# Kernel optimization log

Measured on AMD Instinct MI355X. Metric: run time of the kernel, lower is better.

## Reference

```python
import jax, jax.numpy as jnp
import numpy as np


def setup_inputs() -> dict:
    key = jax.random.key(0)
    k1, k2, k3, k4 = jax.random.split(key, 4)
    b, c, h, w = 4, 256, 64, 64
    Fq_l = jax.random.normal(k1, (b, c, h, w), dtype=jnp.float32)
    Fp_l = jax.random.normal(k2, (b, c, h, w), dtype=jnp.float32)
    # 1x1 conv: weight [out=c//2, in=c], bias [c//2]
    W = jax.random.normal(k3, (c // 2, c), dtype=jnp.float32) * (1.0 / np.sqrt(c))
    bias = jax.random.normal(k4, (c // 2,), dtype=jnp.float32) * 0.01
    return {"Fq_l": Fq_l, "Fp_l": Fp_l, "W": W, "bias": bias}


def reference(Fq_l, Fp_l, W, bias):
    b, c, h, w = Fq_l.shape
    hw = h * w
    # 1x1 conv == per-pixel linear projection
    q = jnp.einsum('oc,bchw->bohw', W, Fq_l) + bias[None, :, None, None]
    p = jnp.einsum('oc,bchw->bohw', W, Fp_l) + bias[None, :, None, None]
    qf = q.reshape(b, -1, hw)  # [b, c/2, hw]
    pf = p.reshape(b, -1, hw)
    qf = qf / jnp.linalg.norm(qf, axis=1, keepdims=True)
    pf = pf / jnp.linalg.norm(pf, axis=1, keepdims=True)
    # cosine similarity, [b, hw, hw]
    sim = jnp.einsum('bcn,bcm->bnm', qf, pf)
    idx = jnp.argmax(sim, axis=-1)  # [b, hw]
    Fp_flat = Fp_l.reshape(b, c, hw)
    aligned = jnp.take_along_axis(Fp_flat, idx[:, None, :], axis=2)  # [b, c, hw]
    return aligned.reshape(b, c, h, w)
```

## Files before the change

kernel.cpp:

```cpp
#include <hip/hip_runtime.h>

#define HW 4096
#define BCAP 1024u
#define OCAP 65536u

typedef short bf16x8 __attribute__((ext_vector_type(8)));
typedef float f32x16 __attribute__((ext_vector_type(16)));

__device__ __forceinline__ ushort f2bf_rne(float f) {
    unsigned u = __float_as_uint(f);
    return (ushort)((u + 0x7FFFu + ((u >> 16) & 1u)) >> 16);
}

__global__ __launch_bounds__(256) void init_kernel(
    unsigned long long* __restrict__ best, unsigned* __restrict__ bcnt,
    unsigned* __restrict__ ocnt)
{
    int i = blockIdx.x * 256 + threadIdx.x;
    best[i] = 0ull;
    if (i < 512) bcnt[i] = 0u;
    if (i == 0) ocnt[0] = 0u;
}

__global__ __launch_bounds__(256) void transpose_w_kernel(
    const float* __restrict__ Wm, float* __restrict__ Wt)
{
    const int o = blockIdx.x;
    const int c = threadIdx.x;
    Wt[c * 128 + o] = Wm[o * 256 + c];
}

__global__ __launch_bounds__(256) void proj_kernel(
    const float* __restrict__ Fq, const float* __restrict__ Fp,
    const float* __restrict__ Wt, const float* __restrict__ bias,
    float* __restrict__ Qt, float* __restrict__ Pt,
    ushort* __restrict__ Qpk, ushort* __restrict__ Ppk,
    float* __restrict__ qnorm)
{
    __shared__ float Ws[64][128];
    __shared__ float Xs[64][64];
    __shared__ float psum[16][68];

    const int tid = threadIdx.x;
    const int z  = blockIdx.z;
    const float* __restrict__ X = z ? Fp : Fq;
    const int b  = blockIdx.y;
    const int n0 = blockIdx.x * 64;
    const int og = tid >> 4;
    const int ng = tid & 15;

    float acc[4][8];
    #pragma unroll
    for (int i = 0; i < 4; ++i)
        #pragma unroll
        for (int j = 0; j < 8; ++j) acc[i][j] = 0.f;

    for (int cc = 0; cc < 4; ++cc) {
        __syncthreads();
        {
            const float4* src = (const float4*)(Wt + (size_t)cc * 64 * 128);
            float4* dst = (float4*)Ws;
            #pragma unroll
            for (int it = 0; it < 8; ++it) dst[it * 256 + tid] = src[it * 256 + tid];
        }
        #pragma unroll
        for (int it = 0; it < 4; ++it) {
            int f = it * 256 + tid;
            int r = f >> 4, n4 = f & 15;
            *(float4*)&Xs[r][n4 * 4] =
                *(const float4*)&X[(size_t)(b * 256 + cc * 64 + r) * HW + n0 + n4 * 4];
        }
        __syncthreads();

        for (int r = 0; r < 64; ++r) {
            float4 w0 = *(const float4*)&Ws[r][og * 8];
            float4 w1 = *(const float4*)&Ws[r][og * 8 + 4];
            float4 xv = *(const float4*)&Xs[r][ng * 4];
            float wa[8] = {w0.x, w0.y, w0.z, w0.w, w1.x, w1.y, w1.z, w1.w};
            float xa[4] = {xv.x, xv.y, xv.z, xv.w};
            #pragma unroll
            for (int i = 0; i < 4; ++i)
                #pragma unroll
                for (int j = 0; j < 8; ++j)
                    acc[i][j] += wa[j] * xa[i];
        }
    }

    {
        float4 b0 = *(const float4*)&bias[og * 8];
        float4 b1 = *(const float4*)&bias[og * 8 + 4];
        float ba[8] = {b0.x, b0.y, b0.z, b0.w, b1.x, b1.y, b1.z, b1.w};
        #pragma unroll
        for (int i = 0; i < 4; ++i)
            #pragma unroll
            for (int j = 0; j < 8; ++j) acc[i][j] += ba[j];
    }

    #pragma unroll
    for (int i = 0; i < 4; ++i) {
        float s = 0.f;
        #pragma unroll
        for (int j = 0; j < 8; ++j) s += acc[i][j] * acc[i][j];
        psum[og][ng * 4 + i] = s;
    }
    __syncthreads();
    float tot[4];
    #pragma unroll
    for (int i = 0; i < 4; ++i) {
        float s = 0.f;
        #pragma unroll
        for (int g = 0; g < 16; ++g) s += psum[g][ng * 4 + i];
        tot[i] = s;
    }

    if (z) {
        #pragma unroll
        for (int i = 0; i < 4; ++i) {
            float s = 1.0f / sqrtf(tot[i]);
            #pragma unroll
            for (int j = 0; j < 8; ++j) acc[i][j] *= s;
        }
    } else if (og == 0) {
        #pragma unroll
        for (int i = 0; i < 4; ++i)
            qnorm[b * HW + n0 + ng * 4 + i] = sqrtf(tot[i]);
    }

    {
        float* __restrict__ T = z ? Pt : Qt;
        #pragma unroll
        for (int i = 0; i < 4; ++i) {
            size_t tb = ((size_t)b * HW + n0 + ng * 4 + i) * 128 + og * 8;
            *(float4*)&T[tb]     = make_float4(acc[i][0], acc[i][1], acc[i][2], acc[i][3]);
            *(float4*)&T[tb + 4] = make_float4(acc[i][4], acc[i][5], acc[i][6], acc[i][7]);
        }
    }
    {
        ushort* __restrict__ PK = z ? Ppk : Qpk;
        const int ks = og >> 1;
        #pragma unroll
        for (int i = 0; i < 4; ++i) {
            const int na  = n0 + ng * 4 + i;
            const int t32 = na >> 5;
            const int lt  = (na & 31) + 32 * (og & 1);
            ushort u[8];
            #pragma unroll
            for (int k = 0; k < 8; ++k) u[k] = f2bf_rne(acc[i][k]);
            size_t pk = ((((size_t)b * 128 + t32) * 8 + ks) * 64 + lt) * 8;
            uint4 w;
            w.x = (unsigned)u[0] | ((unsigned)u[1] << 16);
            w.y = (unsigned)u[2] | ((unsigned)u[3] << 16);
            w.z = (unsigned)u[4] | ((unsigned)u[5] << 16);
            w.w = (unsigned)u[6] | ((unsigned)u[7] << 16);
            *(uint4*)&PK[pk] = w;
        }
    }
}

__global__ __launch_bounds__(256, 2) void sim_max_kernel(
    const ushort* __restrict__ Qpk, const ushort* __restrict__ Ppk,
    float* __restrict__ Vmax)
{
    __shared__ ushort Qs[16384];
    __shared__ ushort Bs[16384];

    const int tid  = threadIdx.x;
    const int lane = tid & 63;
    const int w    = tid >> 6;
    const int nb   = blockIdx.x;
    const int b    = blockIdx.y;
    const int ms   = blockIdx.z;

    {
        const uint4* src = (const uint4*)(Qpk + ((size_t)b * 128 + nb * 4) * 4096);
        uint4* dst = (uint4*)Qs;
        #pragma unroll
        for (int it = 0; it < 8; ++it) dst[it * 256 + tid] = src[it * 256 + tid];
    }

    float bestv[16];
    #pragma unroll
    for (int r = 0; r < 16; ++r) bestv[r] = -1e30f;

    for (int ch = 0; ch < 8; ++ch) {
        __syncthreads();
        {
            const uint4* src = (const uint4*)(Ppk +
                ((size_t)b * 128 + ms * 32 + ch * 4) * 4096);
            uint4* dst = (uint4*)Bs;
            #pragma unroll
            for (int it = 0; it < 8; ++it) dst[it * 256 + tid] = src[it * 256 + tid];
        }
        __syncthreads();

        for (int mtl = 0; mtl < 4; ++mtl) {
            f32x16 acc;
            #pragma unroll
            for (int r = 0; r < 16; ++r) acc[r] = 0.f;
            #pragma unroll
            for (int ks = 0; ks < 8; ++ks) {
                bf16x8 a  = *(const bf16x8*)&Qs[((w   * 8 + ks) * 64 + lane) * 8];
                bf16x8 bb = *(const bf16x8*)&Bs[((mtl * 8 + ks) * 64 + lane) * 8];
                acc = __builtin_amdgcn_mfma_f32_32x32x16_bf16(a, bb, acc, 0, 0, 0);
            }
            #pragma unroll
            for (int r = 0; r < 16; ++r)
                bestv[r] = fmaxf(bestv[r], acc[r]);
        }
    }

    #pragma unroll
    for (int r = 0; r < 16; ++r) {
        float v = bestv[r];
        #pragma unroll
        for (int d = 1; d < 32; d <<= 1)
            v = fmaxf(v, __shfl_xor(v, d, 64));
        if ((lane & 31) == 0) {
            int nl_ = (r & 3) + 8 * (r >> 2) + 4 * (lane >> 5);
            int na = nb * 128 + w * 32 + nl_;
            Vmax[((size_t)b * HW + na) * 4 + ms] = v;
        }
    }
}

__global__ __launch_bounds__(256, 2) void sim_emit_kernel(
    const ushort* __restrict__ Qpk, const ushort* __restrict__ Ppk,
    const float* __restrict__ thr,
    unsigned* __restrict__ cand, unsigned* __restrict__ bcnt,
    unsigned* __restrict__ ocand, unsigned* __restrict__ ocnt)
{
    __shared__ ushort Qs[16384];
    __shared__ ushort Bs[16384];
    __shared__ unsigned lds_cand[BCAP];
    __shared__ unsigned lds_cnt;

    const int tid  = threadIdx.x;
    const int lane = tid & 63;
    const int w    = tid >> 6;
    const int nb   = blockIdx.x;
    const int b    = blockIdx.y;
    const int ms   = blockIdx.z;
    const int blk  = nb + 32 * (b + 4 * ms);

    if (tid == 0) lds_cnt = 0u;

    {
        const uint4* src = (const uint4*)(Qpk + ((size_t)b * 128 + nb * 4) * 4096);
        uint4* dst = (uint4*)Qs;
        #pragma unroll
        for (int it = 0; it < 8; ++it) dst[it * 256 + tid] = src[it * 256 + tid];
    }

    float thrreg[16];
    #pragma unroll
    for (int r = 0; r < 16; ++r) {
        int nl_ = (r & 3) + 8 * (r >> 2) + 4 * (lane >> 5);
        thrreg[r] = thr[b * HW + nb * 128 + w * 32 + nl_];
    }

    for (int ch = 0; ch < 8; ++ch) {
        __syncthreads();
        {
            const uint4* src = (const uint4*)(Ppk +
                ((size_t)b * 128 + ms * 32 + ch * 4) * 4096);
            uint4* dst = (uint4*)Bs;
            #pragma unroll
            for (int it = 0; it < 8; ++it) dst[it * 256 + tid] = src[it * 256 + tid];
        }
        __syncthreads();

        for (int mtl = 0; mtl < 4; ++mtl) {
            f32x16 acc;
            #pragma unroll
            for (int r = 0; r < 16; ++r) acc[r] = 0.f;
            #pragma unroll
            for (int ks = 0; ks < 8; ++ks) {
                bf16x8 a  = *(const bf16x8*)&Qs[((w   * 8 + ks) * 64 + lane) * 8];
                bf16x8 bb = *(const bf16x8*)&Bs[((mtl * 8 + ks) * 64 + lane) * 8];
                acc = __builtin_amdgcn_mfma_f32_32x32x16_bf16(a, bb, acc, 0, 0, 0);
            }

            const int m = ms * 1024 + ch * 128 + mtl * 32 + (lane & 31);
            #pragma unroll
            for (int r = 0; r < 16; ++r) {
                if (acc[r] >= thrreg[r]) {
                    int nl_ = (r & 3) + 8 * (r >> 2) + 4 * (lane >> 5);
                    int na = nb * 128 + w * 32 + nl_;
                    unsigned enc = ((unsigned)b << 24) | ((unsigned)na << 12) | (unsigned)m;
                    unsigned pos = atomicAdd(&lds_cnt, 1u);
                    if (pos < BCAP) {
                        lds_cand[pos] = enc;
                    } else {
                        unsigned op = atomicAdd(ocnt, 1u);
                        if (op < OCAP) ocand[op] = enc;
                    }
                }
            }
        }
    }

    __syncthreads();
    unsigned cnt = lds_cnt;
    if (cnt > BCAP) cnt = BCAP;
    for (unsigned i = tid; i < cnt; i += 256)
        cand[(size_t)blk * BCAP + i] = lds_cand[i];
    if (tid == 0) bcnt[blk] = cnt;
}

__global__ __launch_bounds__(256) void thresh_kernel(
    const float* __restrict__ Vmax, const float* __restrict__ qnorm,
    float* __restrict__ thr)
{
    int i = blockIdx.x * 256 + threadIdx.x;
    float g = -1e30f;
    #pragma unroll
    for (int s = 0; s < 4; ++s) g = fmaxf(g, Vmax[(size_t)i * 4 + s]);
    thr[i] = g - (0.016f * qnorm[i] + 1e-6f);
}

__device__ __forceinline__ void rescore_one(
    const float* __restrict__ Qt, const float* __restrict__ Pt,
    unsigned c, unsigned long long* __restrict__ best)
{
    int m = c & 0xFFF, n = (c >> 12) & 0xFFF, b = c >> 24;
    const float* __restrict__ q = Qt + ((size_t)b * HW + n) * 128;
    const float* __restrict__ p = Pt + ((size_t)b * HW + m) * 128;
    float acc = 0.f;
    for (int k = 0; k < 128; ++k) acc += q[k] * p[k];
    unsigned u = __float_as_uint(acc);
    unsigned kk = (u & 0x80000000u) ? ~u : (u | 0x80000000u);
    unsigned long long key = ((unsigned long long)kk << 32) | (unsigned)(4095 - m);
    atomicMax(&best[(size_t)b * HW + n], key);
}

__global__ __launch_bounds__(256) void rescore_kernel(
    const float* __restrict__ Qt, const float* __restrict__ Pt,
    const unsigned* __restrict__ cand, const unsigned* __restrict__ bcnt,
    const unsigned* __restrict__ ocand, const unsigned* __restrict__ ocnt,
    unsigned long long* __restrict__ best)
{
    const int blk = blockIdx.x;
    const int tid = threadIdx.x;
    unsigned cnt = bcnt[blk];
    for (unsigned i = tid; i < cnt; i += 256)
        rescore_one(Qt, Pt, cand[(size_t)blk * BCAP + i], best);

    unsigned total = ocnt[0];
    if (total > OCAP) total = OCAP;
    for (unsigned i = blk * 256 + tid; i < total; i += 512 * 256)
        rescore_one(Qt, Pt, ocand[i], best);
}

__global__ __launch_bounds__(256) void gather_kernel(
    const float* __restrict__ Fp, const unsigned long long* __restrict__ best,
    float* __restrict__ out)
{
    __shared__ float row[4096];
    const int blk = blockIdx.x;
    const int c = blk & 255;
    const int b = blk >> 8;
    const int tid = threadIdx.x;

    const float* __restrict__ src = Fp + ((size_t)b * 256 + c) * HW;
    #pragma unroll
    for (int it = 0; it < 4; ++it) {
        int f = it * 256 + tid;
        *(float4*)&row[f * 4] = *(const float4*)&src[f * 4];
    }
    __syncthreads();

    float* __restrict__ dst = out + ((size_t)b * 256 + c) * HW;
    #pragma unroll
    for (int it = 0; it < 16; ++it) {
        int n = it * 256 + tid;
        int m = 4095 - (int)(best[(size_t)b * HW + n] & 0xFFFull);
        dst[n] = row[m];
    }
}

extern "C" void kernel_launch(void* const* d_in, const int* in_sizes, int n_in,
                              void* d_out, int out_size, void* d_ws, size_t ws_size,
                              hipStream_t stream) {
    const float* Fq   = (const float*)d_in[0];
    const float* Fp   = (const float*)d_in[1];
    const float* Wm   = (const float*)d_in[2];
    const float* bias = (const float*)d_in[3];
    float* out = (float*)d_out;

    char* base = (char*)d_ws;
    float*  Qt    = (float*)(base);
    float*  Pt    = (float*)(base + (8u << 20));
    ushort* Qpk   = (ushort*)(base + (16u << 20));
    ushort* Ppk   = (ushort*)(base + (20u << 20));
    char* x = base + (24u << 20);
    float*  qnorm = (float*)x;              x += 65536;
    float*  Vmax  = (float*)x;              x += 262144;
    float*  thr   = (float*)x;              x += 65536;
    unsigned long long* best = (unsigned long long*)x; x += 131072;
    unsigned* bcnt = (unsigned*)x;          x += 4096;
    unsigned* ocnt = (unsigned*)x;          x += 16;
    unsigned* cand = (unsigned*)x;          x += (size_t)512 * BCAP * 4;
    unsigned* ocand = (unsigned*)x;         x += OCAP * 4;
    float*  Wtg   = (float*)x;

    init_kernel<<<64, 256, 0, stream>>>(best, bcnt, ocnt);
    transpose_w_kernel<<<128, 256, 0, stream>>>(Wm, Wtg);
    proj_kernel<<<dim3(64, 4, 2), 256, 0, stream>>>(Fq, Fp, Wtg, bias,
                                                    Qt, Pt, Qpk, Ppk, qnorm);
    sim_max_kernel<<<dim3(32, 4, 4), 256, 0, stream>>>(Qpk, Ppk, Vmax);
    thresh_kernel<<<64, 256, 0, stream>>>(Vmax, qnorm, thr);
    sim_emit_kernel<<<dim3(32, 4, 4), 256, 0, stream>>>(Qpk, Ppk, thr,
                                                        cand, bcnt, ocand, ocnt);
    rescore_kernel<<<512, 256, 0, stream>>>(Qt, Pt, cand, bcnt, ocand, ocnt, best);
    gather_kernel<<<1024, 256, 0, stream>>>(Fp, best, out);
}
```

Baseline: 180.4 us.

## Replace second similarity GEMM pass with stored column-group maxima scan

The max pass now also writes, for each 16-row group and column, a bf16 upper bound (rounded up) of the column's maximum similarity. A new scan kernel compares these against the group's minimum threshold to emit candidate columns, so the second full bf16 GEMM pass (sim_emit) is dropped. Rescoring then works per row group, with Q rows staged in LDS and each candidate column tested against all 16 rows, keeping only those above each row's threshold. This trades the second GEMM for an extra 8 MB Cmax write and read, plus a coarser candidate set that may hold more rescoring work per group.

```diff
diff --git a/kernel.cpp b/kernel.cpp
--- a/kernel.cpp
+++ b/kernel.cpp
@@ -1,7 +1,7 @@
 #include <hip/hip_runtime.h>
 
 #define HW 4096
-#define BCAP 1024u
+#define GCAP 512u
 #define OCAP 65536u
 
 typedef short bf16x8 __attribute__((ext_vector_type(8)));
@@ -12,13 +12,20 @@
     return (ushort)((u + 0x7FFFu + ((u >> 16) & 1u)) >> 16);
 }
 
+__device__ __forceinline__ ushort f2bf_up(float f) {
+    unsigned u = __float_as_uint(f);
+    ushort t = (ushort)(u >> 16);
+    if (!(u & 0x80000000u) && (u & 0xFFFFu)) t += 1;
+    return t;
+}
+
 __global__ __launch_bounds__(256) void init_kernel(
-    unsigned long long* __restrict__ best, unsigned* __restrict__ bcnt,
+    unsigned long long* __restrict__ best, unsigned* __restrict__ gcnt,
     unsigned* __restrict__ ocnt)
 {
     int i = blockIdx.x * 256 + threadIdx.x;
     best[i] = 0ull;
-    if (i < 512) bcnt[i] = 0u;
+    if (i < 1024) gcnt[i] = 0u;
     if (i == 0) ocnt[0] = 0u;
 }
 
@@ -159,7 +166,7 @@
 
 __global__ __launch_bounds__(256, 2) void sim_max_kernel(
     const ushort* __restrict__ Qpk, const ushort* __restrict__ Ppk,
-    float* __restrict__ Vmax)
+    float* __restrict__ Vmax, ushort* __restrict__ Cmax)
 {
     __shared__ ushort Qs[16384];
     __shared__ ushort Bs[16384];
@@ -178,6 +185,9 @@
         for (int it = 0; it < 8; ++it) dst[it * 256 + tid] = src[it * 256 + tid];
     }
 
+    const size_t crow = ((size_t)b * 256 + (size_t)(nb * 4 + w) * 2 + (lane >> 5)) * 4096;
+    const int mb0 = ms * 1024 + (lane & 31);
+
     float bestv[16];
     #pragma unroll
     for (int r = 0; r < 16; ++r) bestv[r] = -1e30f;
@@ -206,6 +216,12 @@
             #pragma unroll
             for (int r = 0; r < 16; ++r)
                 bestv[r] = fmaxf(bestv[r], acc[r]);
+
+            float c0 = fmaxf(fmaxf(fmaxf(acc[0], acc[1]), fmaxf(acc[2], acc[3])),
+                             fmaxf(fmaxf(acc[4], acc[5]), fmaxf(acc[6], acc[7])));
+            float c1 = fmaxf(fmaxf(fmaxf(acc[8], acc[9]), fmaxf(acc[10], acc[11])),
+                             fmaxf(fmaxf(acc[12], acc[13]), fmaxf(acc[14], acc[15])));
+            Cmax[crow + mb0 + ch * 128 + mtl * 32] = f2bf_up(fmaxf(c0, c1));
         }
     }
 
@@ -223,76 +239,66 @@
     }
 }
 
-__global__ __launch_bounds__(256, 2) void sim_emit_kernel(
-    const ushort* __restrict__ Qpk, const ushort* __restrict__ Ppk,
-    const float* __restrict__ thr,
-    unsigned* __restrict__ cand, unsigned* __restrict__ bcnt,
+__global__ __launch_bounds__(256) void thresh_kernel(
+    const float* __restrict__ Vmax, const float* __restrict__ qnorm,
+    float* __restrict__ thr, float* __restrict__ gmin)
+{
+    __shared__ float red[256];
+    const int tid = threadIdx.x;
+    int i = blockIdx.x * 256 + tid;
+    float g = -1e30f;
+    #pragma unroll
+    for (int s = 0; s < 4; ++s) g = fmaxf(g, Vmax[(size_t)i * 4 + s]);
+    float t = g - (0.016f * qnorm[i] + 1e-6f);
+    thr[i] = t;
+    red[tid] = t;
+    __syncthreads();
+    if (tid < 16) {
+        int tile = tid >> 1, gs = tid & 1;
+        float mn = 1e30f;
+        #pragma unroll
+        for (int j = 0; j < 16; ++j) {
+            int nl = (j & 3) + 8 * (j >> 2) + 4 * gs;
+            mn = fminf(mn, red[tile * 32 + nl]);
+        }
+        gmin[blockIdx.x * 16 + tid] = mn;
+    }
+}
+
+__global__ __launch_bounds__(256) void scan_kernel(
+    const ushort* __restrict__ Cmax, const float* __restrict__ gmin,
+    unsigned* __restrict__ cand2, unsigned* __restrict__ gcnt,
     unsigned* __restrict__ ocand, unsigned* __restrict__ ocnt)
 {
-    __shared__ ushort Qs[16384];
-    __shared__ ushort Bs[16384];
-    __shared__ unsigned lds_cand[BCAP];
-    __shared__ unsigned lds_cnt;
-
-    const int tid  = threadIdx.x;
-    const int lane = tid & 63;
-    const int w    = tid >> 6;
-    const int nb   = blockIdx.x;
-    const int b    = blockIdx.y;
-    const int ms   = blockIdx.z;
-    const int blk  = nb + 32 * (b + 4 * ms);
-
-    if (tid == 0) lds_cnt = 0u;
-
-    {
-        const uint4* src = (const uint4*)(Qpk + ((size_t)b * 128 + nb * 4) * 4096);
-        uint4* dst = (uint4*)Qs;
-        #pragma unroll
-        for (int it = 0; it < 8; ++it) dst[it * 256 + tid] = src[it * 256 + tid];
-    }
-
-    float thrreg[16];
-    #pragma unroll
-    for (int r = 0; r < 16; ++r) {
-        int nl_ = (r & 3) + 8 * (r >> 2) + 4 * (lane >> 5);
-        thrreg[r] = thr[b * HW + nb * 128 + w * 32 + nl_];
-    }
-
-    for (int ch = 0; ch < 8; ++ch) {
-        __syncthreads();
-        {
-            const uint4* src = (const uint4*)(Ppk +
-                ((size_t)b * 128 + ms * 32 + ch * 4) * 4096);
-            uint4* dst = (uint4*)Bs;
-            #pragma unroll
-            for (int it = 0; it < 8; ++it) dst[it * 256 + tid] = src[it * 256 + tid];
-        }
-        __syncthreads();
-
-        for (int mtl = 0; mtl < 4; ++mtl) {
-            f32x16 acc;
-            #pragma unroll
-            for (int r = 0; r < 16; ++r) acc[r] = 0.f;
-            #pragma unroll
-            for (int ks = 0; ks < 8; ++ks) {
-                bf16x8 a  = *(const bf16x8*)&Qs[((w   * 8 + ks) * 64 + lane) * 8];
-                bf16x8 bb = *(const bf16x8*)&Bs[((mtl * 8 + ks) * 64 + lane) * 8];
-                acc = __builtin_amdgcn_mfma_f32_32x32x16_bf16(a, bb, acc, 0, 0, 0);
-            }
-
-            const int m = ms * 1024 + ch * 128 + mtl * 32 + (lane & 31);
-            #pragma unroll
-            for (int r = 0; r < 16; ++r) {
-                if (acc[r] >= thrreg[r]) {
-                    int nl_ = (r & 3) + 8 * (r >> 2) + 4 * (lane >> 5);
-                    int na = nb * 128 + w * 32 + nl_;
-                    unsigned enc = ((unsigned)b << 24) | ((unsigned)na << 12) | (unsigned)m;
-                    unsigned pos = atomicAdd(&lds_cnt, 1u);
-                    if (pos < BCAP) {
-                        lds_cand[pos] = enc;
+    __shared__ unsigned lcnt;
+    const int fg = blockIdx.x;
+    const int tid = threadIdx.x;
+    if (tid == 0) lcnt = 0u;
+    __syncthreads();
+
+    const float gm = gmin[fg];
+    const ushort* __restrict__ row = Cmax + (size_t)fg * 4096;
+
+    #pragma unroll
+    for (int it = 0; it < 4; ++it) {
+        int m0 = (it * 256 + tid) * 4;
+        uint2 v = *(const uint2*)&row[m0];
+        unsigned wv[2] = {v.x, v.y};
+        #pragma unroll
+        for (int h = 0; h < 2; ++h) {
+            float f0 = __uint_as_float((wv[h] & 0xFFFFu) << 16);
+            float f1 = __uint_as_float(wv[h] & 0xFFFF0000u);
+            #pragma unroll
+            for (int q = 0; q < 2; ++q) {
+                float f = q ? f1 : f0;
+                if (f >= gm) {
+                    unsigned m = (unsigned)(m0 + h * 2 + q);
+                    unsigned pos = atomicAdd(&lcnt, 1u);
+                    if (pos < GCAP) {
+                        cand2[(size_t)fg * GCAP + pos] = m;
                     } else {
                         unsigned op = atomicAdd(ocnt, 1u);
-                        if (op < OCAP) ocand[op] = enc;
+                        if (op < OCAP) ocand[op] = ((unsigned)fg << 12) | m;
                     }
                 }
             }
@@ -300,55 +306,78 @@
     }
 
     __syncthreads();
-    unsigned cnt = lds_cnt;
-    if (cnt > BCAP) cnt = BCAP;
-    for (unsigned i = tid; i < cnt; i += 256)
-        cand[(size_t)blk * BCAP + i] = lds_cand[i];
-    if (tid == 0) bcnt[blk] = cnt;
-}
-
-__global__ __launch_bounds__(256) void thresh_kernel(
-    const float* __restrict__ Vmax, const float* __restrict__ qnorm,
-    float* __restrict__ thr)
-{
-    int i = blockIdx.x * 256 + threadIdx.x;
-    float g = -1e30f;
-    #pragma unroll
-    for (int s = 0; s < 4; ++s) g = fmaxf(g, Vmax[(size_t)i * 4 + s]);
-    thr[i] = g - (0.016f * qnorm[i] + 1e-6f);
-}
-
-__device__ __forceinline__ void rescore_one(
-    const float* __restrict__ Qt, const float* __restrict__ Pt,
-    unsigned c, unsigned long long* __restrict__ best)
-{
-    int m = c & 0xFFF, n = (c >> 12) & 0xFFF, b = c >> 24;
-    const float* __restrict__ q = Qt + ((size_t)b * HW + n) * 128;
-    const float* __restrict__ p = Pt + ((size_t)b * HW + m) * 128;
-    float acc = 0.f;
-    for (int k = 0; k < 128; ++k) acc += q[k] * p[k];
-    unsigned u = __float_as_uint(acc);
-    unsigned kk = (u & 0x80000000u) ? ~u : (u | 0x80000000u);
-    unsigned long long key = ((unsigned long long)kk << 32) | (unsigned)(4095 - m);
-    atomicMax(&best[(size_t)b * HW + n], key);
+    if (tid == 0) gcnt[fg] = lcnt < GCAP ? lcnt : GCAP;
 }
 
 __global__ __launch_bounds__(256) void rescore_kernel(
     const float* __restrict__ Qt, const float* __restrict__ Pt,
-    const unsigned* __restrict__ cand, const unsigned* __restrict__ bcnt,
+    const float* __restrict__ thr,
+    const unsigned* __restrict__ cand2, const unsigned* __restrict__ gcnt,
     const unsigned* __restrict__ ocand, const unsigned* __restrict__ ocnt,
     unsigned long long* __restrict__ best)
 {
-    const int blk = blockIdx.x;
+    __shared__ float Qs[16][132];
+    __shared__ float thr_s[16];
+    __shared__ int nlist[16];
+
+    const int fg = blockIdx.x;
     const int tid = threadIdx.x;
-    unsigned cnt = bcnt[blk];
-    for (unsigned i = tid; i < cnt; i += 256)
-        rescore_one(Qt, Pt, cand[(size_t)blk * BCAP + i], best);
+    const int b = fg >> 8, g = fg & 255, t = g >> 1, gs = g & 1;
+
+    if (tid < 16) {
+        int n = t * 32 + (tid & 3) + 8 * (tid >> 2) + 4 * gs;
+        nlist[tid] = n;
+        thr_s[tid] = thr[b * HW + n];
+    }
+    __syncthreads();
+    #pragma unroll
+    for (int it = 0; it < 2; ++it) {
+        int idx = it * 256 + tid;
+        int row = idx >> 5, c4 = (idx & 31) * 4;
+        *(float4*)&Qs[row][c4] =
+            *(const float4*)&Qt[((size_t)b * HW + nlist[row]) * 128 + c4];
+    }
+    __syncthreads();
+
+    unsigned cnt = gcnt[fg];
+    for (unsigned p = tid; p < cnt * 16u; p += 256) {
+        unsigned i = p >> 4, sub = p & 15;
+        int m = (int)cand2[(size_t)fg * GCAP + i];
+        const float4* __restrict__ pr = (const float4*)&Pt[((size_t)b * HW + m) * 128];
+        float acc = 0.f;
+        #pragma unroll
+        for (int k = 0; k < 32; ++k) {
+            float4 pv = pr[k];
+            float4 qv = *(const float4*)&Qs[sub][k * 4];
+            acc += qv.x * pv.x + qv.y * pv.y + qv.z * pv.z + qv.w * pv.w;
+        }
+        if (acc >= thr_s[sub]) {
+            unsigned u = __float_as_uint(acc);
+            unsigned kk = (u & 0x80000000u) ? ~u : (u | 0x80000000u);
+            unsigned long long key = ((unsigned long long)kk << 32) | (unsigned)(4095 - m);
+            atomicMax(&best[(size_t)b * HW + nlist[sub]], key);
+        }
+    }
 
     unsigned total = ocnt[0];
     if (total > OCAP) total = OCAP;
-    for (unsigned i = blk * 256 + tid; i < total; i += 512 * 256)
-        rescore_one(Qt, Pt, ocand[i], best);
+    for (unsigned i = blockIdx.x * 256 + tid; i < total; i += 1024 * 256) {
+        unsigned e = ocand[i];
+        unsigned fg2 = e >> 12, m = e & 4095u;
+        int b2 = fg2 >> 8, g2 = fg2 & 255, t2 = g2 >> 1, gs2 = g2 & 1;
+        const float* __restrict__ prow = &Pt[((size_t)b2 * HW + m) * 128];
+        #pragma unroll 1
+        for (int j = 0; j < 16; ++j) {
+            int n = t2 * 32 + (j & 3) + 8 * (j >> 2) + 4 * gs2;
+            const float* __restrict__ q = &Qt[((size_t)b2 * HW + n) * 128];
+            float acc = 0.f;
+            for (int k = 0; k < 128; ++k) acc += q[k] * prow[k];
+            unsigned u = __float_as_uint(acc);
+            unsigned kk = (u & 0x80000000u) ? ~u : (u | 0x80000000u);
+            unsigned long long key = ((unsigned long long)kk << 32) | (unsigned)(4095 - m);
+            atomicMax(&best[(size_t)b2 * HW + n], key);
+        }
+    }
 }
 
 __global__ __launch_bounds__(256) void gather_kernel(
@@ -392,25 +421,27 @@
     float*  Pt    = (float*)(base + (8u << 20));
     ushort* Qpk   = (ushort*)(base + (16u << 20));
     ushort* Ppk   = (ushort*)(base + (20u << 20));
-    char* x = base + (24u << 20);
+    ushort* Cmax  = (ushort*)(base + (24u << 20));
+    char* x = base + (32u << 20);
     float*  qnorm = (float*)x;              x += 65536;
     float*  Vmax  = (float*)x;              x += 262144;
     float*  thr   = (float*)x;              x += 65536;
+    float*  gmin  = (float*)x;              x += 4096;
     unsigned long long* best = (unsigned long long*)x; x += 131072;
-    unsigned* bcnt = (unsigned*)x;          x += 4096;
-    unsigned* ocnt = (unsigned*)x;          x += 16;
-    unsigned* cand = (unsigned*)x;          x += (size_t)512 * BCAP * 4;
+    unsigned* gcnt = (unsigned*)x;          x += 4096;
+    unsigned* ocnt = (unsigned*)x;          x += 4096;
+    unsigned* cand2 = (unsigned*)x;         x += (size_t)1024 * GCAP * 4;
     unsigned* ocand = (unsigned*)x;         x += OCAP * 4;
     float*  Wtg   = (float*)x;
 
-    init_kernel<<<64, 256, 0, stream>>>(best, bcnt, ocnt);
+    init_kernel<<<64, 256, 0, stream>>>(best, gcnt, ocnt);
     transpose_w_kernel<<<128, 256, 0, stream>>>(Wm, Wtg);
     proj_kernel<<<dim3(64, 4, 2), 256, 0, stream>>>(Fq, Fp, Wtg, bias,
                                                     Qt, Pt, Qpk, Ppk, qnorm);
-    sim_max_kernel<<<dim3(32, 4, 4), 256, 0, stream>>>(Qpk, Ppk, Vmax);
-    thresh_kernel<<<64, 256, 0, stream>>>(Vmax, qnorm, thr);
-    sim_emit_kernel<<<dim3(32, 4, 4), 256, 0, stream>>>(Qpk, Ppk, thr,
-                                                        cand, bcnt, ocand, ocnt);
-    rescore_kernel<<<512, 256, 0, stream>>>(Qt, Pt, cand, bcnt, ocand, ocnt, best);
+    sim_max_kernel<<<dim3(32, 4, 4), 256, 0, stream>>>(Qpk, Ppk, Vmax, Cmax);
+    thresh_kernel<<<64, 256, 0, stream>>>(Vmax, qnorm, thr, gmin);
+    scan_kernel<<<1024, 256, 0, stream>>>(Cmax, gmin, cand2, gcnt, ocand, ocnt);
+    rescore_kernel<<<1024, 256, 0, stream>>>(Qt, Pt, thr, cand2, gcnt,
+                                             ocand, ocnt, best);
     gather_kernel<<<1024, 256, 0, stream>>>(Fp, best, out);
 }
```

Result: slower. 363.0 us (+101.2%).
